# Kernel optimization log

Hardware: AMD Instinct MI355X
Metric: run time of the kernel (lower is better)

The kernel has to match this reference:

```python
import jax, jax.numpy as jnp
import numpy as np

HID, NBINS = 256, 4
NMIR, NMRNA, B, NP, PD = 2000, 20000, 16, 2048, 1024
EREG, EPM, EPI = 300000, 320000, 32000


def _lin(x, w, b):
    return x @ w.T + b


def _gelu(x):
    # torch nn.GELU default = exact erf formulation
    return jax.nn.gelu(x, approximate=False)


def _ln(x, g, b):
    m = jnp.mean(x, axis=-1, keepdims=True)
    v = jnp.mean((x - m) ** 2, axis=-1, keepdims=True)
    return (x - m) * jax.lax.rsqrt(v + 1e-5) * g + b


def setup_inputs() -> dict:
    key = jax.random.key(0)
    ks = jax.random.split(key, 48)

    def lin_w(i, dout, din):
        s = 1.0 / np.sqrt(din)
        return jax.random.uniform(ks[i], (dout, din), minval=-s, maxval=s, dtype=jnp.float32)

    inp = {}
    inp['emb_mirna'] = jax.random.normal(ks[0], (NMIR, HID), jnp.float32) * 0.02
    inp['emb_mrna'] = jax.random.normal(ks[1], (NMRNA, HID), jnp.float32) * 0.02
    inp['w_mir2mrna'] = jax.random.uniform(ks[2], (EREG,), jnp.float32)
    inp['w_mrna2mir'] = jax.random.uniform(ks[3], (EREG,), jnp.float32)
    inp['w_mrna2pat'] = jax.random.uniform(ks[4], (EPM,), jnp.float32)
    inp['w_mir2pat'] = jax.random.uniform(ks[5], (EPI,), jnp.float32)
    inp['reg_w_mrna'] = lin_w(6, HID, HID)
    inp['reg_b_mrna'] = jnp.zeros((HID,), jnp.float32)
    inp['reg_w_mirna'] = lin_w(7, HID, HID)
    inp['reg_b_mirna'] = jnp.zeros((HID,), jnp.float32)
    inp['proj_w'] = lin_w(8, HID, HID)
    inp['proj_b'] = jnp.zeros((HID,), jnp.float32)
    inp['ln_g'] = jnp.ones((HID,), jnp.float32)
    inp['ln_b'] = jnp.zeros((HID,), jnp.float32)
    inp['omics_w'] = lin_w(9, NBINS, HID)
    inp['omics_b'] = jnp.zeros((NBINS,), jnp.float32)
    inp['wsi_w'] = lin_w(10, HID, PD)
    inp['wsi_b'] = jnp.zeros((HID,), jnp.float32)
    inp['mlp_w'] = lin_w(11, HID, HID)
    inp['mlp_b'] = jnp.zeros((HID,), jnp.float32)
    inp['wln_g'] = jnp.ones((HID,), jnp.float32)
    inp['wln_b'] = jnp.zeros((HID,), jnp.float32)
    inp['fuse_w1'] = lin_w(12, HID, 2 * HID)
    inp['fuse_b1'] = jnp.zeros((HID,), jnp.float32)
    inp['fuse_w2'] = lin_w(13, NBINS, HID)
    inp['fuse_b2'] = jnp.zeros((NBINS,), jnp.float32)
    inp['patches'] = jax.random.normal(ks[14], (B, NP, PD), jnp.float32)
    inp['mask'] = jnp.ones((B, NP), jnp.float32)
    inp['src_mir2mrna'] = jax.random.randint(ks[15], (EREG,), 0, NMIR, jnp.int32)
    inp['dst_mir2mrna'] = jax.random.randint(ks[16], (EREG,), 0, NMRNA, jnp.int32)
    inp['src_mrna2mir'] = jax.random.randint(ks[17], (EREG,), 0, NMRNA, jnp.int32)
    inp['dst_mrna2mir'] = jax.random.randint(ks[18], (EREG,), 0, NMIR, jnp.int32)
    inp['src_mrna2pat'] = jax.random.randint(ks[19], (EPM,), 0, NMRNA, jnp.int32)
    inp['dst_mrna2pat'] = jax.random.randint(ks[20], (EPM,), 0, B, jnp.int32)
    inp['src_mir2pat'] = jax.random.randint(ks[21], (EPI,), 0, NMIR, jnp.int32)
    inp['dst_mir2pat'] = jax.random.randint(ks[22], (EPI,), 0, B, jnp.int32)
    return inp


def reference(emb_mirna, emb_mrna, w_mir2mrna, w_mrna2mir, w_mrna2pat, w_mir2pat,
              reg_w_mrna, reg_b_mrna, reg_w_mirna, reg_b_mirna,
              proj_w, proj_b, ln_g, ln_b, omics_w, omics_b,
              wsi_w, wsi_b, mlp_w, mlp_b, wln_g, wln_b,
              fuse_w1, fuse_b1, fuse_w2, fuse_b2, patches, mask,
              src_mir2mrna, dst_mir2mrna, src_mrna2mir, dst_mrna2mir,
              src_mrna2pat, dst_mrna2pat, src_mir2pat, dst_mir2pat):
    # ---- omics: node embeddings (nid = arange -> full tables) ----
    h_mir, h_mrna = emb_mirna, emb_mrna
    # ---- SimpleRegEncoder: weighted gather-scatter-sum per etype (on ORIGINAL h) ----
    agg_mrna = jax.ops.segment_sum(h_mir[src_mir2mrna] * w_mir2mrna[:, None], dst_mir2mrna, num_segments=NMRNA)
    agg_mir = jax.ops.segment_sum(h_mrna[src_mrna2mir] * w_mrna2mir[:, None], dst_mrna2mir, num_segments=NMIR)
    h_mrna = h_mrna + _gelu(_lin(agg_mrna, reg_w_mrna, reg_b_mrna))  # dropout = identity (eval)
    h_mir = h_mir + _gelu(_lin(agg_mir, reg_w_mirna, reg_b_mirna))
    # ---- PatientReadout: cross_reducer='sum' over both gene->patient etypes ----
    acc = (jax.ops.segment_sum(h_mrna[src_mrna2pat] * w_mrna2pat[:, None], dst_mrna2pat, num_segments=B)
           + jax.ops.segment_sum(h_mir[src_mir2pat] * w_mir2pat[:, None], dst_mir2pat, num_segments=B))
    pat = _ln(_gelu(_lin(acc, proj_w, proj_b)), ln_g, ln_b)  # [B, HID]
    omics_logits = _lin(pat, omics_w, omics_b)  # [B, NBINS]
    # ---- SimpleWSIEncoder ----
    x = _lin(patches, wsi_w, wsi_b)  # [B, NP, HID]
    denom = jnp.clip(jnp.sum(mask, axis=1, keepdims=True), 1.0, None)
    pooled = jnp.sum(x * mask[:, :, None], axis=1) / denom
    pooled = _gelu(_lin(_gelu(pooled), mlp_w, mlp_b))
    wsi = _ln(pooled, wln_g, wln_b)  # [B, HID]
    # ---- fusion head ----
    cat = jnp.concatenate([pat, wsi], axis=-1)  # [B, 2*HID]
    fused = _lin(_gelu(_lin(cat, fuse_w1, fuse_b1)), fuse_w2, fuse_b2)  # [B, NBINS]
    return fused, omics_logits
```

## Files before the change

kernel.cpp:

```cpp
#include <hip/hip_runtime.h>
#include <math.h>

#define HID 256
#define NBINS 4
#define NMIR 2000
#define NMRNA 20000
#define NG (NMRNA + NMIR)
#define BB 16
#define NP 2048
#define PD 1024
#define EREG 300000
#define EPM 320000
#define EPI 32000

typedef __attribute__((ext_vector_type(8))) short bf16x8;
typedef __attribute__((ext_vector_type(4))) float f32x4;

__device__ __forceinline__ float gelu_exact(float x) {
    return 0.5f * x * (1.0f + erff(x * 0.7071067811865475f));
}

__device__ __forceinline__ unsigned short f2b(float f) {
    union { float f; unsigned int u; } v; v.f = f;
    unsigned int u = v.u + 0x7fffu + ((v.u >> 16) & 1u);
    return (unsigned short)(u >> 16);
}

__device__ __forceinline__ float b2f(unsigned short u) {
    union { unsigned int i; float f; } v; v.i = ((unsigned int)u) << 16;
    return v.f;
}

__device__ __forceinline__ float block_reduce_sum(float v, float* red) {
    int c = threadIdx.x;
    red[c] = v;
    __syncthreads();
    for (int st = 128; st > 0; st >>= 1) {
        if (c < st) red[c] += red[c + st];
        __syncthreads();
    }
    float r = red[0];
    __syncthreads();
    return r;
}

__device__ __forceinline__ float kred(float v, float* red, int b, int kk) {
    red[kk * 16 + b] = v;
    __syncthreads();
    for (int st = 8; st >= 1; st >>= 1) {
        if (kk < st) red[kk * 16 + b] += red[(kk + st) * 16 + b];
        __syncthreads();
    }
    float r = red[b];
    __syncthreads();
    return r;
}

#define MISC_POOL 512
#define PSLICES 32
#define PCHUNK (NP / PSLICES)
#define MISC_EMB (((NMIR + NMRNA) * HID) / 1024)
#define MISC_HIST ((2 * EREG + 255) / 256)
#define MISC_WSC ((EPM + EPI + 255) / 256)
#define MISC_F2B ((2 * HID * HID) / 1024)
#define MISC_TOTAL (MISC_POOL + MISC_EMB + MISC_HIST + MISC_WSC + MISC_F2B)

__global__ __launch_bounds__(256) void k_misc(
        const float* __restrict__ patches, const float* __restrict__ mask,
        float* __restrict__ pooled, float* __restrict__ masksum,
        const float* __restrict__ emb_mirna, const float* __restrict__ emb_mrna,
        unsigned short* __restrict__ embB_mir, unsigned short* __restrict__ embB_mrna,
        const int* __restrict__ dA, const int* __restrict__ dB, int* __restrict__ cnt,
        const int* __restrict__ srcP, const int* __restrict__ dstP, const float* __restrict__ wP,
        const int* __restrict__ srcI, const int* __restrict__ dstI, const float* __restrict__ wI,
        float* __restrict__ Wp,
        const float* __restrict__ regwA, const float* __restrict__ regwB,
        unsigned short* __restrict__ wb) {
    int bid = blockIdx.x;
    int t = threadIdx.x;
    if (bid < MISC_POOL) {
        int slice = bid & 31, b = bid >> 5;
        int p0 = slice * PCHUNK;
        float4 acc = {0.f, 0.f, 0.f, 0.f};
        float msum = 0.f;
        for (int p = p0; p < p0 + PCHUNK; p++) {
            float m = mask[b * NP + p];
            msum += m;
            float4 v = ((const float4*)(patches + ((size_t)b * NP + p) * PD))[t];
            acc.x += m * v.x; acc.y += m * v.y; acc.z += m * v.z; acc.w += m * v.w;
        }
        float* op = pooled + (size_t)b * PD + t * 4;
        atomicAdd(op + 0, acc.x);
        atomicAdd(op + 1, acc.y);
        atomicAdd(op + 2, acc.z);
        atomicAdd(op + 3, acc.w);
        if (t == 0) atomicAdd(&masksum[b], msum);
        return;
    }
    bid -= MISC_POOL;
    if (bid < MISC_EMB) {
        size_t e = (size_t)bid * 1024 + t * 4;
        const size_t NM = (size_t)NMIR * HID;
        float4 v;
        unsigned short* o;
        if (e < NM) { v = *(const float4*)(emb_mirna + e); o = embB_mir + e; }
        else        { v = *(const float4*)(emb_mrna + (e - NM)); o = embB_mrna + (e - NM); }
        ushort4 u = { f2b(v.x), f2b(v.y), f2b(v.z), f2b(v.w) };
        *(ushort4*)o = u;
        return;
    }
    bid -= MISC_EMB;
    if (bid < MISC_HIST) {
        int i = bid * 256 + t;
        if (i < EREG) atomicAdd(&cnt[dA[i]], 1);
        else if (i < 2 * EREG) atomicAdd(&cnt[NMRNA + dB[i - EREG]], 1);
        return;
    }
    bid -= MISC_HIST;
    if (bid < MISC_WSC) {
        int i = bid * 256 + t;
        if (i < EPM) {
            atomicAdd(&Wp[(size_t)dstP[i] * NG + srcP[i]], wP[i]);
        } else if (i < EPM + EPI) {
            int j = i - EPM;
            atomicAdd(&Wp[(size_t)dstI[j] * NG + NMRNA + srcI[j]], wI[j]);
        }
        return;
    }
    bid -= MISC_WSC;
    {
        size_t e = (size_t)bid * 1024 + t * 4;
        float4 v;
        if (e < (size_t)HID * HID) v = *(const float4*)(regwA + e);
        else v = *(const float4*)(regwB + (e - HID * HID));
        ushort4 u = { f2b(v.x), f2b(v.y), f2b(v.z), f2b(v.w) };
        *(ushort4*)(wb + e) = u;
    }
}

__global__ __launch_bounds__(1024) void k_scan2(const int* __restrict__ cnt,
                                                int* __restrict__ rpA, int* __restrict__ cuA,
                                                int* __restrict__ rpB, int* __restrict__ cuB) {
    __shared__ int part[1024];
    const int* c = (blockIdx.x == 0) ? cnt : cnt + NMRNA;
    int n = (blockIdx.x == 0) ? NMRNA : NMIR;
    int* rowptr = (blockIdx.x == 0) ? rpA : rpB;
    int* cursor = (blockIdx.x == 0) ? cuA : cuB;
    int t = threadIdx.x;
    int chunk = (n + 1023) >> 10;
    int beg = t * chunk;
    int end = min(beg + chunk, n);
    int s = 0;
    for (int i = beg; i < end; i++) s += c[i];
    part[t] = s;
    __syncthreads();
    for (int st = 1; st < 1024; st <<= 1) {
        int v = (t >= st) ? part[t - st] : 0;
        __syncthreads();
        part[t] += v;
        __syncthreads();
    }
    int off = part[t] - s;
    for (int i = beg; i < end; i++) {
        rowptr[i] = off;
        cursor[i] = off;
        off += c[i];
    }
    if (end == n) rowptr[n] = off;
}

__global__ void k_place2(
        const int* __restrict__ srcA, const int* __restrict__ dstA, const float* __restrict__ wA,
        int* __restrict__ cuA, int* __restrict__ srcpA, float* __restrict__ wpA,
        const int* __restrict__ srcB, const int* __restrict__ dstB, const float* __restrict__ wB,
        int* __restrict__ cuB, int* __restrict__ srcpB, float* __restrict__ wpB) {
    int i = blockIdx.x * blockDim.x + threadIdx.x;
    if (i < EREG) {
        int p = atomicAdd(&cuA[dstA[i]], 1);
        srcpA[p] = srcA[i];
        wpA[p] = wA[i];
    } else if (i < 2 * EREG) {
        int j = i - EREG;
        int p = atomicAdd(&cuB[dstB[j]], 1);
        srcpB[p] = srcB[j];
        wpB[p] = wB[j];
    }
}

__global__ __launch_bounds__(256) void k_gather2(
        const unsigned short* __restrict__ embB_mir, const unsigned short* __restrict__ embB_mrna,
        const int* __restrict__ rpA, const int* __restrict__ srcpA, const float* __restrict__ wpA,
        const int* __restrict__ rpB, const int* __restrict__ srcpB, const float* __restrict__ wpB,
        unsigned short* __restrict__ agg) {
    __shared__ float lacc[4][HID];
    int n = blockIdx.x;
    const unsigned short* emb;
    const int* rp; const int* srcp; const float* wp;
    int node;
    if (n < NMRNA) { emb = embB_mir;  rp = rpA; srcp = srcpA; wp = wpA; node = n; }
    else           { emb = embB_mrna; rp = rpB; srcp = srcpB; wp = wpB; node = n - NMRNA; }
    int wv = threadIdx.x >> 6, l = threadIdx.x & 63;
    int beg = rp[node], end = rp[node + 1];
    float a0 = 0.f, a1 = 0.f, a2 = 0.f, a3 = 0.f;
    for (int j = beg + wv; j < end; j += 4) {
        int s = srcp[j];
        float we = wp[j];
        ushort4 v = *(const ushort4*)(emb + (size_t)s * HID + l * 4);
        a0 += we * b2f(v.x);
        a1 += we * b2f(v.y);
        a2 += we * b2f(v.z);
        a3 += we * b2f(v.w);
    }
    float4 st = { a0, a1, a2, a3 };
    ((float4*)lacc[wv])[l] = st;
    __syncthreads();
    int c = threadIdx.x;
    agg[(size_t)n * HID + c] = f2b(lacc[0][c] + lacc[1][c] + lacc[2][c] + lacc[3][c]);
}

__global__ __launch_bounds__(256) void k_update2(
        const unsigned short* __restrict__ A,
        const float* __restrict__ emb_mrna, const float* __restrict__ emb_mirna,
        const unsigned short* __restrict__ wb,
        const float* __restrict__ bias_mrna, const float* __restrict__ bias_mirna,
        const float* __restrict__ Wp, float* __restrict__ acc_pat) {
    __shared__ float ht[16][HID + 1];
    int row0 = blockIdx.x * 16;
    const float* emb; const unsigned short* Wb; const float* bias; int base;
    if (row0 < NMRNA) { emb = emb_mrna;  Wb = wb;             bias = bias_mrna;  base = 0; }
    else              { emb = emb_mirna; Wb = wb + HID * HID; bias = bias_mirna; base = NMRNA; }
    int wv = threadIdx.x >> 6;
    int lane = threadIdx.x & 63;
    int m = lane & 15;
    int q = lane >> 4;
    bf16x8 afrag[8];
    const unsigned short* arow = A + (size_t)(row0 + m) * HID + q * 8;
#pragma unroll
    for (int kk = 0; kk < 8; kk++)
        afrag[kk] = *(const bf16x8*)(arow + kk * 32);
    f32x4 acc[4];
#pragma unroll
    for (int t = 0; t < 4; t++) acc[t] = (f32x4){0.f, 0.f, 0.f, 0.f};
    int col_base = wv * 64;
#pragma unroll
    for (int t = 0; t < 4; t++) {
        const unsigned short* brow = Wb + (size_t)(col_base + t * 16 + m) * HID + q * 8;
#pragma unroll
        for (int kk = 0; kk < 8; kk++) {
            bf16x8 bfrag = *(const bf16x8*)(brow + kk * 32);
            acc[t] = __builtin_amdgcn_mfma_f32_16x16x32_bf16(afrag[kk], bfrag, acc[t], 0, 0, 0);
        }
    }
#pragma unroll
    for (int t = 0; t < 4; t++) {
        int col = col_base + t * 16 + m;
        float bv = bias[col];
#pragma unroll
        for (int r = 0; r < 4; r++) {
            int lrow = q * 4 + r;
            size_t idxe = (size_t)(row0 - base + lrow) * HID + col;
            ht[lrow][col] = emb[idxe] + gelu_exact(acc[t][r] + bv);
        }
    }
    __syncthreads();
    int c = threadIdx.x;
    float hv[16];
#pragma unroll
    for (int r = 0; r < 16; r++) hv[r] = ht[r][c];
#pragma unroll
    for (int b = 0; b < BB; b++) {
        const float* wpr = Wp + (size_t)b * NG + row0;
        float s = 0.f;
#pragma unroll
        for (int r = 0; r < 16; r++) s += wpr[r] * hv[r];
        atomicAdd(&acc_pat[b * HID + c], s);
    }
}

__global__ __launch_bounds__(256) void k_head_a(
        const float* __restrict__ acc_pat, const float* __restrict__ pooled,
        const float* __restrict__ masksum,
        const float* __restrict__ proj_w, const float* __restrict__ proj_b,
        const float* __restrict__ wsi_w, const float* __restrict__ wsi_b,
        float* __restrict__ pg, float* __restrict__ wt) {
    __shared__ float red[256];
    int c = blockIdx.x;
    int t = threadIdx.x;
    int b = t & 15, kk = t >> 4;

    const float* wr = proj_w + (size_t)c * HID + kk * 16;
    const float* xr = acc_pat + (size_t)b * HID + kk * 16;
    float s = 0.f;
#pragma unroll
    for (int i = 0; i < 16; i += 4) {
        float4 w4 = *(const float4*)(wr + i);
        float4 x4 = *(const float4*)(xr + i);
        s += x4.x * w4.x + x4.y * w4.y + x4.z * w4.z + x4.w * w4.w;
    }
    float tot = kred(s, red, b, kk);
    if (kk == 0) pg[(size_t)b * HID + c] = gelu_exact(tot + proj_b[c]);

    const float* wr2 = wsi_w + (size_t)c * PD + kk * 64;
    const float* xr2 = pooled + (size_t)b * PD + kk * 64;
    float s2 = 0.f;
#pragma unroll
    for (int i = 0; i < 64; i += 4) {
        float4 w4 = *(const float4*)(wr2 + i);
        float4 x4 = *(const float4*)(xr2 + i);
        s2 += x4.x * w4.x + x4.y * w4.y + x4.z * w4.z + x4.w * w4.w;
    }
    float tot2 = kred(s2, red, b, kk);
    if (kk == 0) {
        float sm = masksum[b];
        float denom = fmaxf(sm, 1.0f);
        wt[(size_t)b * HID + c] = gelu_exact(tot2 / denom + wsi_b[c] * (sm / denom));
    }
}

__global__ __launch_bounds__(256) void k_head_b(
        const float* __restrict__ wt,
        const float* __restrict__ mlp_w, const float* __restrict__ mlp_b,
        float* __restrict__ ml) {
    __shared__ float red[256];
    int c = blockIdx.x;
    int t = threadIdx.x;
    int b = t & 15, kk = t >> 4;
    const float* wr = mlp_w + (size_t)c * HID + kk * 16;
    const float* xr = wt + (size_t)b * HID + kk * 16;
    float s = 0.f;
#pragma unroll
    for (int i = 0; i < 16; i += 4) {
        float4 w4 = *(const float4*)(wr + i);
        float4 x4 = *(const float4*)(xr + i);
        s += x4.x * w4.x + x4.y * w4.y + x4.z * w4.z + x4.w * w4.w;
    }
    float tot = kred(s, red, b, kk);
    if (kk == 0) ml[(size_t)b * HID + c] = gelu_exact(tot + mlp_b[c]);
}

__global__ __launch_bounds__(256) void k_head_c(
        const float* __restrict__ pg, const float* __restrict__ ml,
        const float* __restrict__ ln_g, const float* __restrict__ ln_b,
        const float* __restrict__ wln_g, const float* __restrict__ wln_b,
        const float* __restrict__ omics_w, const float* __restrict__ omics_b,
        const float* __restrict__ fuse_b2,
        float* __restrict__ vecbuf, float* __restrict__ out_omics,
        float* __restrict__ out_fused) {
    __shared__ float red[256];
    int b = blockIdx.x, c = threadIdx.x;
    if (c < NBINS) out_fused[b * NBINS + c] = fuse_b2[c];
    float g = pg[(size_t)b * HID + c];
    float mean = block_reduce_sum(g, red) * (1.0f / HID);
    float d = g - mean;
    float var = block_reduce_sum(d * d, red) * (1.0f / HID);
    float patv = d * rsqrtf(var + 1e-5f) * ln_g[c] + ln_b[c];
    vecbuf[(size_t)b * (2 * HID) + c] = patv;
    for (int o = 0; o < NBINS; o++) {
        float r = block_reduce_sum(patv * omics_w[o * HID + c], red);
        if (c == 0) out_omics[b * NBINS + o] = r + omics_b[o];
    }
    float m = ml[(size_t)b * HID + c];
    mean = block_reduce_sum(m, red) * (1.0f / HID);
    d = m - mean;
    var = block_reduce_sum(d * d, red) * (1.0f / HID);
    vecbuf[(size_t)b * (2 * HID) + HID + c] = d * rsqrtf(var + 1e-5f) * wln_g[c] + wln_b[c];
}

__global__ __launch_bounds__(256) void k_head_d(
        const float* __restrict__ vecbuf,
        const float* __restrict__ fuse_w1, const float* __restrict__ fuse_b1,
        const float* __restrict__ fuse_w2,
        float* __restrict__ out_fused) {
    __shared__ float red[256];
    int c = blockIdx.x;
    int t = threadIdx.x;
    int b = t & 15, kk = t >> 4;
    const float* wr = fuse_w1 + (size_t)c * (2 * HID) + kk * 32;
    const float* xr = vecbuf + (size_t)b * (2 * HID) + kk * 32;
    float s = 0.f;
#pragma unroll
    for (int i = 0; i < 32; i += 4) {
        float4 w4 = *(const float4*)(wr + i);
        float4 x4 = *(const float4*)(xr + i);
        s += x4.x * w4.x + x4.y * w4.y + x4.z * w4.z + x4.w * w4.w;
    }
    float tot = kred(s, red, b, kk);
    if (kk == 0) {
        float h1 = gelu_exact(tot + fuse_b1[c]);
#pragma unroll
        for (int o = 0; o < NBINS; o++)
            atomicAdd(&out_fused[b * NBINS + o], h1 * fuse_w2[o * HID + c]);
    }
}

extern "C" void kernel_launch(void* const* d_in, const int* in_sizes, int n_in,
                              void* d_out, int out_size, void* d_ws, size_t ws_size,
                              hipStream_t stream) {
    const float* emb_mirna  = (const float*)d_in[0];
    const float* emb_mrna   = (const float*)d_in[1];
    const float* w_mir2mrna = (const float*)d_in[2];
    const float* w_mrna2mir = (const float*)d_in[3];
    const float* w_mrna2pat = (const float*)d_in[4];
    const float* w_mir2pat  = (const float*)d_in[5];
    const float* reg_w_mrna = (const float*)d_in[6];
    const float* reg_b_mrna = (const float*)d_in[7];
    const float* reg_w_mirna= (const float*)d_in[8];
    const float* reg_b_mirna= (const float*)d_in[9];
    const float* proj_w     = (const float*)d_in[10];
    const float* proj_b     = (const float*)d_in[11];
    const float* ln_g       = (const float*)d_in[12];
    const float* ln_b       = (const float*)d_in[13];
    const float* omics_w    = (const float*)d_in[14];
    const float* omics_b    = (const float*)d_in[15];
    const float* wsi_w      = (const float*)d_in[16];
    const float* wsi_b      = (const float*)d_in[17];
    const float* mlp_w      = (const float*)d_in[18];
    const float* mlp_b      = (const float*)d_in[19];
    const float* wln_g      = (const float*)d_in[20];
    const float* wln_b      = (const float*)d_in[21];
    const float* fuse_w1    = (const float*)d_in[22];
    const float* fuse_b1    = (const float*)d_in[23];
    const float* fuse_w2    = (const float*)d_in[24];
    const float* fuse_b2    = (const float*)d_in[25];
    const float* patches    = (const float*)d_in[26];
    const float* mask       = (const float*)d_in[27];
    const int* src_m2M = (const int*)d_in[28];
    const int* dst_m2M = (const int*)d_in[29];
    const int* src_M2m = (const int*)d_in[30];
    const int* dst_M2m = (const int*)d_in[31];
    const int* src_M2p = (const int*)d_in[32];
    const int* dst_M2p = (const int*)d_in[33];
    const int* src_m2p = (const int*)d_in[34];
    const int* dst_m2p = (const int*)d_in[35];

    float* ws = (float*)d_ws;
    size_t off = 0;
    float* acc_pat  = ws + off; off += (size_t)BB * HID;
    float* pooled   = ws + off; off += (size_t)BB * PD;
    float* Wp       = ws + off; off += (size_t)BB * NG;
    int* cnt        = (int*)(ws + off); off += NG;
    float* masksum  = ws + off; off += BB;
    size_t zero_floats = off;
    unsigned short* agg_bf = (unsigned short*)(ws + off); off += (size_t)NG * HID / 2;
    unsigned short* wb     = (unsigned short*)(ws + off); off += (size_t)2 * HID * HID / 2;
    unsigned short* embB_mir  = (unsigned short*)(ws + off); off += (size_t)NMIR * HID / 2;
    unsigned short* embB_mrna = (unsigned short*)(ws + off); off += (size_t)NMRNA * HID / 2;
    float* pg       = ws + off; off += (size_t)BB * HID;
    float* wt       = ws + off; off += (size_t)BB * HID;
    float* ml       = ws + off; off += (size_t)BB * HID;
    float* vecbuf   = ws + off; off += (size_t)BB * 2 * HID;
    int* rowptr_A   = (int*)(ws + off); off += NMRNA + 1;
    int* cursor_A   = (int*)(ws + off); off += NMRNA;
    int* rowptr_B   = (int*)(ws + off); off += NMIR + 1;
    int* cursor_B   = (int*)(ws + off); off += NMIR;
    int* srcp_A     = (int*)(ws + off); off += EREG;
    float* wp_A     = ws + off; off += EREG;
    int* srcp_B     = (int*)(ws + off); off += EREG;
    float* wp_B     = ws + off; off += EREG;

    float* out_fused = (float*)d_out;
    float* out_omics = (float*)d_out + BB * NBINS;

    hipMemsetAsync(d_ws, 0, zero_floats * sizeof(float), stream);

    k_misc<<<MISC_TOTAL, 256, 0, stream>>>(
        patches, mask, pooled, masksum,
        emb_mirna, emb_mrna, embB_mir, embB_mrna,
        dst_m2M, dst_M2m, cnt,
        src_M2p, dst_M2p, w_mrna2pat, src_m2p, dst_m2p, w_mir2pat, Wp,
        reg_w_mrna, reg_w_mirna, wb);

    k_scan2<<<2, 1024, 0, stream>>>(cnt, rowptr_A, cursor_A, rowptr_B, cursor_B);
    k_place2<<<(2 * EREG + 255) / 256, 256, 0, stream>>>(
        src_m2M, dst_m2M, w_mir2mrna, cursor_A, srcp_A, wp_A,
        src_M2m, dst_M2m, w_mrna2mir, cursor_B, srcp_B, wp_B);

    k_gather2<<<NG, 256, 0, stream>>>(embB_mir, embB_mrna,
                                      rowptr_A, srcp_A, wp_A,
                                      rowptr_B, srcp_B, wp_B, agg_bf);

    k_update2<<<NG / 16, 256, 0, stream>>>(agg_bf, emb_mrna, emb_mirna, wb,
                                           reg_b_mrna, reg_b_mirna, Wp, acc_pat);

    k_head_a<<<HID, 256, 0, stream>>>(acc_pat, pooled, masksum,
                                      proj_w, proj_b, wsi_w, wsi_b, pg, wt);
    k_head_b<<<HID, 256, 0, stream>>>(wt, mlp_w, mlp_b, ml);
    k_head_c<<<BB, 256, 0, stream>>>(pg, ml, ln_g, ln_b, wln_g, wln_b,
                                     omics_w, omics_b, fuse_b2,
                                     vecbuf, out_omics, out_fused);
    k_head_d<<<HID, 256, 0, stream>>>(vecbuf, fuse_w1, fuse_b1, fuse_w2, out_fused);
}
```

Before: 597.0 us.

## Split patch pooling into its own kernel, pack edge pairs, unroll gather

Moves the masked patch pooling out of the combined misc kernel into a dedicated 2D-grid kernel with four times as many slices and an unrolled inner loop, raising the parallelism on the largest memory stream (128 MB of patches). Edge source index and weight are packed into a single int2 array, so the gather does one 8-byte load per edge instead of two separate loads. The gather loop is also unrolled by two with independent accumulators to keep more loads in flight. The cost is an extra kernel launch and more atomics into the pooled buffer.

```diff
diff --git a/kernel.cpp b/kernel.cpp
--- a/kernel.cpp
+++ b/kernel.cpp
@@ -56,49 +56,24 @@
     return r;
 }
 
-#define MISC_POOL 512
-#define PSLICES 32
-#define PCHUNK (NP / PSLICES)
-#define MISC_EMB (((NMIR + NMRNA) * HID) / 1024)
-#define MISC_HIST ((2 * EREG + 255) / 256)
-#define MISC_WSC ((EPM + EPI + 255) / 256)
-#define MISC_F2B ((2 * HID * HID) / 1024)
-#define MISC_TOTAL (MISC_POOL + MISC_EMB + MISC_HIST + MISC_WSC + MISC_F2B)
-
-__global__ __launch_bounds__(256) void k_misc(
-        const float* __restrict__ patches, const float* __restrict__ mask,
-        float* __restrict__ pooled, float* __restrict__ masksum,
+#define M2_EMB (((NMIR + NMRNA) * HID) / 1024)
+#define M2_F2B ((2 * HID * HID) / 1024)
+#define M2_HIST ((2 * EREG + 255) / 256)
+#define M2_WSC ((EPM + EPI + 255) / 256)
+#define M2_TOTAL (M2_EMB + M2_F2B + M2_HIST + M2_WSC)
+
+__global__ __launch_bounds__(256) void k_misc2(
         const float* __restrict__ emb_mirna, const float* __restrict__ emb_mrna,
         unsigned short* __restrict__ embB_mir, unsigned short* __restrict__ embB_mrna,
+        const float* __restrict__ regwA, const float* __restrict__ regwB,
+        unsigned short* __restrict__ wb,
         const int* __restrict__ dA, const int* __restrict__ dB, int* __restrict__ cnt,
         const int* __restrict__ srcP, const int* __restrict__ dstP, const float* __restrict__ wP,
         const int* __restrict__ srcI, const int* __restrict__ dstI, const float* __restrict__ wI,
-        float* __restrict__ Wp,
-        const float* __restrict__ regwA, const float* __restrict__ regwB,
-        unsigned short* __restrict__ wb) {
+        float* __restrict__ Wp) {
     int bid = blockIdx.x;
     int t = threadIdx.x;
-    if (bid < MISC_POOL) {
-        int slice = bid & 31, b = bid >> 5;
-        int p0 = slice * PCHUNK;
-        float4 acc = {0.f, 0.f, 0.f, 0.f};
-        float msum = 0.f;
-        for (int p = p0; p < p0 + PCHUNK; p++) {
-            float m = mask[b * NP + p];
-            msum += m;
-            float4 v = ((const float4*)(patches + ((size_t)b * NP + p) * PD))[t];
-            acc.x += m * v.x; acc.y += m * v.y; acc.z += m * v.z; acc.w += m * v.w;
-        }
-        float* op = pooled + (size_t)b * PD + t * 4;
-        atomicAdd(op + 0, acc.x);
-        atomicAdd(op + 1, acc.y);
-        atomicAdd(op + 2, acc.z);
-        atomicAdd(op + 3, acc.w);
-        if (t == 0) atomicAdd(&masksum[b], msum);
-        return;
-    }
-    bid -= MISC_POOL;
-    if (bid < MISC_EMB) {
+    if (bid < M2_EMB) {
         size_t e = (size_t)bid * 1024 + t * 4;
         const size_t NM = (size_t)NMIR * HID;
         float4 v;
@@ -109,15 +84,25 @@
         *(ushort4*)o = u;
         return;
     }
-    bid -= MISC_EMB;
-    if (bid < MISC_HIST) {
+    bid -= M2_EMB;
+    if (bid < M2_F2B) {
+        size_t e = (size_t)bid * 1024 + t * 4;
+        float4 v;
+        if (e < (size_t)HID * HID) v = *(const float4*)(regwA + e);
+        else v = *(const float4*)(regwB + (e - HID * HID));
+        ushort4 u = { f2b(v.x), f2b(v.y), f2b(v.z), f2b(v.w) };
+        *(ushort4*)(wb + e) = u;
+        return;
+    }
+    bid -= M2_F2B;
+    if (bid < M2_HIST) {
         int i = bid * 256 + t;
         if (i < EREG) atomicAdd(&cnt[dA[i]], 1);
         else if (i < 2 * EREG) atomicAdd(&cnt[NMRNA + dB[i - EREG]], 1);
         return;
     }
-    bid -= MISC_HIST;
-    if (bid < MISC_WSC) {
+    bid -= M2_HIST;
+    {
         int i = bid * 256 + t;
         if (i < EPM) {
             atomicAdd(&Wp[(size_t)dstP[i] * NG + srcP[i]], wP[i]);
@@ -125,17 +110,33 @@
             int j = i - EPM;
             atomicAdd(&Wp[(size_t)dstI[j] * NG + NMRNA + srcI[j]], wI[j]);
         }
-        return;
-    }
-    bid -= MISC_WSC;
-    {
-        size_t e = (size_t)bid * 1024 + t * 4;
-        float4 v;
-        if (e < (size_t)HID * HID) v = *(const float4*)(regwA + e);
-        else v = *(const float4*)(regwB + (e - HID * HID));
-        ushort4 u = { f2b(v.x), f2b(v.y), f2b(v.z), f2b(v.w) };
-        *(ushort4*)(wb + e) = u;
-    }
+    }
+}
+
+#define PSLICES 128
+#define PCHUNK (NP / PSLICES)
+__global__ __launch_bounds__(256) void k_pool(
+        const float* __restrict__ patches, const float* __restrict__ mask,
+        float* __restrict__ pooled, float* __restrict__ masksum) {
+    int b = blockIdx.y;
+    int p0 = blockIdx.x * PCHUNK;
+    int t = threadIdx.x;
+    float4 acc = {0.f, 0.f, 0.f, 0.f};
+    float msum = 0.f;
+#pragma unroll
+    for (int pp = 0; pp < PCHUNK; pp++) {
+        int p = p0 + pp;
+        float m = mask[b * NP + p];
+        float4 v = ((const float4*)(patches + ((size_t)b * NP + p) * PD))[t];
+        msum += m;
+        acc.x += m * v.x; acc.y += m * v.y; acc.z += m * v.z; acc.w += m * v.w;
+    }
+    float* op = pooled + (size_t)b * PD + t * 4;
+    atomicAdd(op + 0, acc.x);
+    atomicAdd(op + 1, acc.y);
+    atomicAdd(op + 2, acc.z);
+    atomicAdd(op + 3, acc.w);
+    if (t == 0) atomicAdd(&masksum[b], msum);
 }
 
 __global__ __launch_bounds__(1024) void k_scan2(const int* __restrict__ cnt,
@@ -171,47 +172,56 @@
 
 __global__ void k_place2(
         const int* __restrict__ srcA, const int* __restrict__ dstA, const float* __restrict__ wA,
-        int* __restrict__ cuA, int* __restrict__ srcpA, float* __restrict__ wpA,
+        int* __restrict__ cuA, int2* __restrict__ epA,
         const int* __restrict__ srcB, const int* __restrict__ dstB, const float* __restrict__ wB,
-        int* __restrict__ cuB, int* __restrict__ srcpB, float* __restrict__ wpB) {
+        int* __restrict__ cuB, int2* __restrict__ epB) {
     int i = blockIdx.x * blockDim.x + threadIdx.x;
     if (i < EREG) {
         int p = atomicAdd(&cuA[dstA[i]], 1);
-        srcpA[p] = srcA[i];
-        wpA[p] = wA[i];
+        int2 e; e.x = srcA[i]; e.y = __float_as_int(wA[i]);
+        epA[p] = e;
     } else if (i < 2 * EREG) {
         int j = i - EREG;
         int p = atomicAdd(&cuB[dstB[j]], 1);
-        srcpB[p] = srcB[j];
-        wpB[p] = wB[j];
+        int2 e; e.x = srcB[j]; e.y = __float_as_int(wB[j]);
+        epB[p] = e;
     }
 }
 
 __global__ __launch_bounds__(256) void k_gather2(
         const unsigned short* __restrict__ embB_mir, const unsigned short* __restrict__ embB_mrna,
-        const int* __restrict__ rpA, const int* __restrict__ srcpA, const float* __restrict__ wpA,
-        const int* __restrict__ rpB, const int* __restrict__ srcpB, const float* __restrict__ wpB,
+        const int* __restrict__ rpA, const int2* __restrict__ epA,
+        const int* __restrict__ rpB, const int2* __restrict__ epB,
         unsigned short* __restrict__ agg) {
     __shared__ float lacc[4][HID];
     int n = blockIdx.x;
     const unsigned short* emb;
-    const int* rp; const int* srcp; const float* wp;
+    const int* rp; const int2* ep;
     int node;
-    if (n < NMRNA) { emb = embB_mir;  rp = rpA; srcp = srcpA; wp = wpA; node = n; }
-    else           { emb = embB_mrna; rp = rpB; srcp = srcpB; wp = wpB; node = n - NMRNA; }
+    if (n < NMRNA) { emb = embB_mir;  rp = rpA; ep = epA; node = n; }
+    else           { emb = embB_mrna; rp = rpB; ep = epB; node = n - NMRNA; }
     int wv = threadIdx.x >> 6, l = threadIdx.x & 63;
     int beg = rp[node], end = rp[node + 1];
     float a0 = 0.f, a1 = 0.f, a2 = 0.f, a3 = 0.f;
-    for (int j = beg + wv; j < end; j += 4) {
-        int s = srcp[j];
-        float we = wp[j];
-        ushort4 v = *(const ushort4*)(emb + (size_t)s * HID + l * 4);
-        a0 += we * b2f(v.x);
-        a1 += we * b2f(v.y);
-        a2 += we * b2f(v.z);
-        a3 += we * b2f(v.w);
-    }
-    float4 st = { a0, a1, a2, a3 };
+    float c0 = 0.f, c1 = 0.f, c2 = 0.f, c3 = 0.f;
+    int j = beg + wv;
+    for (; j + 4 < end; j += 8) {
+        int2 e0 = ep[j];
+        int2 e1 = ep[j + 4];
+        float w0 = __int_as_float(e0.y);
+        float w1 = __int_as_float(e1.y);
+        ushort4 v0 = *(const ushort4*)(emb + (size_t)e0.x * HID + l * 4);
+        ushort4 v1 = *(const ushort4*)(emb + (size_t)e1.x * HID + l * 4);
+        a0 += w0 * b2f(v0.x); a1 += w0 * b2f(v0.y); a2 += w0 * b2f(v0.z); a3 += w0 * b2f(v0.w);
+        c0 += w1 * b2f(v1.x); c1 += w1 * b2f(v1.y); c2 += w1 * b2f(v1.z); c3 += w1 * b2f(v1.w);
+    }
+    if (j < end) {
+        int2 e0 = ep[j];
+        float w0 = __int_as_float(e0.y);
+        ushort4 v0 = *(const ushort4*)(emb + (size_t)e0.x * HID + l * 4);
+        a0 += w0 * b2f(v0.x); a1 += w0 * b2f(v0.y); a2 += w0 * b2f(v0.z); a3 += w0 * b2f(v0.w);
+    }
+    float4 st = { a0 + c0, a1 + c1, a2 + c2, a3 + c3 };
     ((float4*)lacc[wv])[l] = st;
     __syncthreads();
     int c = threadIdx.x;
@@ -449,35 +459,33 @@
     float* wt       = ws + off; off += (size_t)BB * HID;
     float* ml       = ws + off; off += (size_t)BB * HID;
     float* vecbuf   = ws + off; off += (size_t)BB * 2 * HID;
+    int2* epA       = (int2*)(ws + off); off += (size_t)2 * EREG;
+    int2* epB       = (int2*)(ws + off); off += (size_t)2 * EREG;
     int* rowptr_A   = (int*)(ws + off); off += NMRNA + 1;
     int* cursor_A   = (int*)(ws + off); off += NMRNA;
     int* rowptr_B   = (int*)(ws + off); off += NMIR + 1;
     int* cursor_B   = (int*)(ws + off); off += NMIR;
-    int* srcp_A     = (int*)(ws + off); off += EREG;
-    float* wp_A     = ws + off; off += EREG;
-    int* srcp_B     = (int*)(ws + off); off += EREG;
-    float* wp_B     = ws + off; off += EREG;
 
     float* out_fused = (float*)d_out;
     float* out_omics = (float*)d_out + BB * NBINS;
 
     hipMemsetAsync(d_ws, 0, zero_floats * sizeof(float), stream);
 
-    k_misc<<<MISC_TOTAL, 256, 0, stream>>>(
-        patches, mask, pooled, masksum,
+    k_misc2<<<M2_TOTAL, 256, 0, stream>>>(
         emb_mirna, emb_mrna, embB_mir, embB_mrna,
+        reg_w_mrna, reg_w_mirna, wb,
         dst_m2M, dst_M2m, cnt,
-        src_M2p, dst_M2p, w_mrna2pat, src_m2p, dst_m2p, w_mir2pat, Wp,
-        reg_w_mrna, reg_w_mirna, wb);
+        src_M2p, dst_M2p, w_mrna2pat, src_m2p, dst_m2p, w_mir2pat, Wp);
+
+    k_pool<<<dim3(PSLICES, BB), 256, 0, stream>>>(patches, mask, pooled, masksum);
 
     k_scan2<<<2, 1024, 0, stream>>>(cnt, rowptr_A, cursor_A, rowptr_B, cursor_B);
     k_place2<<<(2 * EREG + 255) / 256, 256, 0, stream>>>(
-        src_m2M, dst_m2M, w_mir2mrna, cursor_A, srcp_A, wp_A,
-        src_M2m, dst_M2m, w_mrna2mir, cursor_B, srcp_B, wp_B);
+        src_m2M, dst_m2M, w_mir2mrna, cursor_A, epA,
+        src_M2m, dst_M2m, w_mrna2mir, cursor_B, epB);
 
     k_gather2<<<NG, 256, 0, stream>>>(embB_mir, embB_mrna,
-                                      rowptr_A, srcp_A, wp_A,
-                                      rowptr_B, srcp_B, wp_B, agg_bf);
+                                      rowptr_A, epA, rowptr_B, epB, agg_bf);
 
     k_update2<<<NG / 16, 256, 0, stream>>>(agg_bf, emb_mrna, emb_mirna, wb,
                                            reg_b_mrna, reg_b_mirna, Wp, acc_pat);
```

Result: no change. 605.7 us (+1.5%).
